# Performance work log

Measured on AMD Instinct MI355X. Metric: run time of the kernel, lower is better.

The kernel has to match this reference:

```python
import jax, jax.numpy as jnp
import numpy as np

D_MODEL = 1024
NUM_HEADS = 16
D_K = D_MODEL // NUM_HEADS


def setup_inputs() -> dict:
    key = jax.random.key(0)
    ks = jax.random.split(key, 11)
    B, S = 2, 2048
    scale = 1.0 / np.sqrt(D_MODEL)
    inp = {
        "query": jax.random.normal(ks[0], (B, S, D_MODEL), jnp.float32),
        "key": jax.random.normal(ks[1], (B, S, D_MODEL), jnp.float32),
        "value": jax.random.normal(ks[2], (B, S, D_MODEL), jnp.float32),
        "Wq": jax.random.normal(ks[3], (D_MODEL, D_MODEL), jnp.float32) * scale,
        "bq": jnp.zeros((D_MODEL,), jnp.float32),
        "Wk": jax.random.normal(ks[4], (D_MODEL, D_MODEL), jnp.float32) * scale,
        "bk": jnp.zeros((D_MODEL,), jnp.float32),
        "Wv": jax.random.normal(ks[5], (D_MODEL, D_MODEL), jnp.float32) * scale,
        "bv": jnp.zeros((D_MODEL,), jnp.float32),
        "Wo": jax.random.normal(ks[6], (D_MODEL, D_MODEL), jnp.float32) * scale,
        "bo": jnp.zeros((D_MODEL,), jnp.float32),
    }
    return inp


def _split_heads(x):
    B, S, _ = x.shape
    return x.reshape(B, S, NUM_HEADS, D_K).transpose(0, 2, 1, 3)  # [B,H,S,d_k]


def reference(query, key, value, Wq, bq, Wk, bk, Wv, bv, Wo, bo):
    # Linear projections (torch Linear: x @ W.T + b)
    q = _split_heads(query @ Wq.T + bq)
    k = _split_heads(key @ Wk.T + bk)
    v = _split_heads(value @ Wv.T + bv)
    scores = jnp.einsum("bhqd,bhkd->bhqk", q, k) / jnp.sqrt(jnp.float32(D_K))
    probs = jax.nn.softmax(scores, axis=-1)
    out = jnp.einsum("bhqk,bhkd->bhqd", probs, v)  # [B,H,S,d_k]
    B, H, S, _ = out.shape
    out = out.transpose(0, 2, 1, 3).reshape(B, S, D_MODEL)
    return out @ Wo.T + bo
```

## Files before the change

### kernel.cpp

```cpp
#include <hip/hip_runtime.h>

#define D_MODEL 1024
#define NHEADS  16
#define DK      64
#define SEQ     2048
#define NBATCH  2
#define MTOT    (NBATCH * SEQ)

typedef _Float16 f16;
typedef _Float16 f16x4 __attribute__((ext_vector_type(4)));
typedef _Float16 f16x8 __attribute__((ext_vector_type(8)));
typedef float    f32x4 __attribute__((ext_vector_type(4)));

__global__ __launch_bounds__(256) void cvt_f32_to_f16(
    const float* __restrict__ q, const float* __restrict__ k, const float* __restrict__ v,
    const float* __restrict__ wq, const float* __restrict__ wk,
    const float* __restrict__ wv, const float* __restrict__ wo,
    f16* __restrict__ qf, f16* __restrict__ kf, f16* __restrict__ vf,
    f16* __restrict__ wqh, f16* __restrict__ wkh, f16* __restrict__ wvh, f16* __restrict__ woh)
{
    const int z = blockIdx.y;
    const float* src; f16* dst; int n4;
    if (z == 0)      { src = q;  dst = qf;  n4 = MTOT * D_MODEL / 4; }
    else if (z == 1) { src = k;  dst = kf;  n4 = MTOT * D_MODEL / 4; }
    else if (z == 2) { src = v;  dst = vf;  n4 = MTOT * D_MODEL / 4; }
    else if (z == 3) { src = wq; dst = wqh; n4 = D_MODEL * D_MODEL / 4; }
    else if (z == 4) { src = wk; dst = wkh; n4 = D_MODEL * D_MODEL / 4; }
    else if (z == 5) { src = wv; dst = wvh; n4 = D_MODEL * D_MODEL / 4; }
    else             { src = wo; dst = woh; n4 = D_MODEL * D_MODEL / 4; }
    for (int i = blockIdx.x * 256 + threadIdx.x; i < n4; i += gridDim.x * 256) {
        float4 t = ((const float4*)src)[i];
        f16x4 o = {(f16)t.x, (f16)t.y, (f16)t.z, (f16)t.w};
        ((f16x4*)dst)[i] = o;
    }
}

__device__ __forceinline__ void gemm128_core(
    const f16* __restrict__ A, const f16* __restrict__ Wm,
    int m0, int n0, f32x4 (&acc)[4][4])
{
    __shared__ __align__(16) f16 As[4096];
    __shared__ __align__(16) f16 Bs[4096];

    const int t    = threadIdx.x;
    const int lane = t & 63;
    const int w    = t >> 6;
    const int quad = lane >> 4, l15 = lane & 15;
    const int wr   = w >> 1,    wc  = w & 1;

    size_t offA[2], offB[2];
#pragma unroll
    for (int jj = 0; jj < 2; ++jj) {
        int s  = (w * 2 + jj) * 64 + lane;
        int ko = s >> 7, m = s & 127;
        offA[jj] = (size_t)(m0 + m) * D_MODEL + ko * 8;
        offB[jj] = (size_t)(n0 + m) * D_MODEL + ko * 8;
    }
    const int jb = __builtin_amdgcn_readfirstlane(w * 2 * 512);

#pragma unroll
    for (int i = 0; i < 4; ++i)
#pragma unroll
        for (int j = 0; j < 4; ++j) acc[i][j] = (f32x4){0.f, 0.f, 0.f, 0.f};

    auto* ldsA = (__attribute__((address_space(3))) f16*)As;
    auto* ldsB = (__attribute__((address_space(3))) f16*)Bs;

    for (int k0 = 0; k0 < D_MODEL; k0 += 32) {
#pragma unroll
        for (int jj = 0; jj < 2; ++jj) {
            __builtin_amdgcn_global_load_lds(
                (const __attribute__((address_space(1))) void*)(A + offA[jj] + k0),
                (__attribute__((address_space(3))) void*)(ldsA + jb + jj * 512),
                16, 0, 0);
            __builtin_amdgcn_global_load_lds(
                (const __attribute__((address_space(1))) void*)(Wm + offB[jj] + k0),
                (__attribute__((address_space(3))) void*)(ldsB + jb + jj * 512),
                16, 0, 0);
        }
        __syncthreads();

        f16x8 af[4], bf[4];
#pragma unroll
        for (int i = 0; i < 4; ++i) {
            af[i] = *(const f16x8*)&As[quad * 1024 + (wr * 64 + i * 16 + l15) * 8];
            bf[i] = *(const f16x8*)&Bs[quad * 1024 + (wc * 64 + i * 16 + l15) * 8];
        }
#pragma unroll
        for (int i = 0; i < 4; ++i)
#pragma unroll
            for (int j = 0; j < 4; ++j)
                acc[i][j] = __builtin_amdgcn_mfma_f32_16x16x32_f16(af[i], bf[j], acc[i][j], 0, 0, 0);
        __syncthreads();
    }
}

__global__ __launch_bounds__(256, 3) void qkv_gemm(
    const f16* __restrict__ Qf, const f16* __restrict__ Kf, const f16* __restrict__ Vf,
    const f16* __restrict__ Wqh, const f16* __restrict__ Wkh, const f16* __restrict__ Wvh,
    const float* __restrict__ bq, const float* __restrict__ bk, const float* __restrict__ bv,
    f16* __restrict__ Qh, f16* __restrict__ Kh, f16* __restrict__ Vt)
{
    const int z = blockIdx.z;
    const f16*   A    = z == 0 ? Qf  : z == 1 ? Kf  : Vf;
    const f16*   Wm   = z == 0 ? Wqh : z == 1 ? Wkh : Wvh;
    const float* bias = z == 0 ? bq  : z == 1 ? bk  : bv;

    const int m0 = blockIdx.y * 128, n0 = blockIdx.x * 128;
    f32x4 acc[4][4];
    gemm128_core(A, Wm, m0, n0, acc);

    const int t = threadIdx.x, lane = t & 63, w = t >> 6;
    const int quad = lane >> 4, l15 = lane & 15;
    const int wr = w >> 1, wc = w & 1;

    if (z < 2) {
        f16* Out = z == 0 ? Qh : Kh;
#pragma unroll
        for (int j = 0; j < 4; ++j) {
            const int col = n0 + wc * 64 + j * 16 + l15;
            const float bc = bias[col];
#pragma unroll
            for (int i = 0; i < 4; ++i)
#pragma unroll
                for (int r = 0; r < 4; ++r) {
                    const int row = m0 + wr * 64 + i * 16 + quad * 4 + r;
                    Out[(size_t)row * D_MODEL + col] = (f16)(acc[i][j][r] + bc);
                }
        }
    } else {
#pragma unroll
        for (int j = 0; j < 4; ++j) {
            const int col = n0 + wc * 64 + j * 16 + l15;
            const float bc = bias[col];
            const int h = col >> 6, d = col & 63;
#pragma unroll
            for (int i = 0; i < 4; ++i)
#pragma unroll
                for (int r = 0; r < 4; ++r) {
                    const int row = m0 + wr * 64 + i * 16 + quad * 4 + r;
                    const int bb = row >> 11, s = row & (SEQ - 1);
                    Vt[(size_t)((bb * NHEADS + h) * DK + d) * SEQ + s] = (f16)(acc[i][j][r] + bc);
                }
        }
    }
}

__global__ __launch_bounds__(256, 3) void oproj_gemm(
    const f16* __restrict__ A, const f16* __restrict__ Wm,
    const float* __restrict__ bias, float* __restrict__ Out)
{
    const int m0 = blockIdx.y * 128, n0 = blockIdx.x * 128;
    f32x4 acc[4][4];
    gemm128_core(A, Wm, m0, n0, acc);

    const int t = threadIdx.x, lane = t & 63, w = t >> 6;
    const int quad = lane >> 4, l15 = lane & 15;
    const int wr = w >> 1, wc = w & 1;
#pragma unroll
    for (int j = 0; j < 4; ++j) {
        const int col = n0 + wc * 64 + j * 16 + l15;
        const float bc = bias[col];
#pragma unroll
        for (int i = 0; i < 4; ++i)
#pragma unroll
            for (int r = 0; r < 4; ++r) {
                const int row = m0 + wr * 64 + i * 16 + quad * 4 + r;
                Out[(size_t)row * D_MODEL + col] = acc[i][j][r] + bc;
            }
    }
}

__global__ __launch_bounds__(256) void mha_mfma_f16(
    const f16* __restrict__ Qh, const f16* __restrict__ Kh,
    const f16* __restrict__ Vt, f16* __restrict__ Og)
{
    __shared__ __align__(16) f16 Qs[64][72];
    __shared__ __align__(16) f16 Ks[64][72];
    __shared__ __align__(16) f16 Vs[64][72];
    __shared__ __align__(16) f16 Ps[64][72];

    const int t    = threadIdx.x;
    const int w    = t >> 6;
    const int lane = t & 63;
    const int quad = lane >> 4;
    const int l15  = lane & 15;

    const int qt = blockIdx.x;
    const int bh = blockIdx.y;
    const int b  = bh >> 4;
    const int h  = bh & 15;
    const int q0 = qt * 64;

    const int r0 = t >> 3;
    const int c0 = (t & 7) * 8;

#pragma unroll
    for (int i = 0; i < 2; ++i) {
        int r = r0 + i * 32;
        *(f16x8*)&Qs[r][c0] =
            *(const f16x8*)&Qh[(size_t)(b * SEQ + q0 + r) * D_MODEL + h * DK + c0];
    }
    __syncthreads();

    const f16x8 aQ0 = *(const f16x8*)&Qs[w * 16 + l15][quad * 8];
    const f16x8 aQ1 = *(const f16x8*)&Qs[w * 16 + l15][32 + quad * 8];

    f32x4 o[4];
#pragma unroll
    for (int f = 0; f < 4; ++f) o[f] = (f32x4){0.f, 0.f, 0.f, 0.f};
    float m_run[4], l_run[4];
#pragma unroll
    for (int r = 0; r < 4; ++r) { m_run[r] = -1e30f; l_run[r] = 0.f; }

    for (int kt = 0; kt < SEQ / 64; ++kt) {
        const int kv0 = kt * 64;
#pragma unroll
        for (int i = 0; i < 2; ++i) {
            int r = r0 + i * 32;
            *(f16x8*)&Ks[r][c0] =
                *(const f16x8*)&Kh[(size_t)(b * SEQ + kv0 + r) * D_MODEL + h * DK + c0];
            *(f16x8*)&Vs[r][c0] =
                *(const f16x8*)&Vt[(size_t)(bh * DK + r) * SEQ + kv0 + c0];
        }
        __syncthreads();

        f32x4 s[4];
#pragma unroll
        for (int f = 0; f < 4; ++f) {
            f16x8 b0 = *(const f16x8*)&Ks[f * 16 + l15][quad * 8];
            f16x8 b1 = *(const f16x8*)&Ks[f * 16 + l15][32 + quad * 8];
            f32x4 a0 = (f32x4){0.f, 0.f, 0.f, 0.f};
            a0 = __builtin_amdgcn_mfma_f32_16x16x32_f16(aQ0, b0, a0, 0, 0, 0);
            a0 = __builtin_amdgcn_mfma_f32_16x16x32_f16(aQ1, b1, a0, 0, 0, 0);
            s[f] = a0;
        }

#pragma unroll
        for (int f = 0; f < 4; ++f)
#pragma unroll
            for (int r = 0; r < 4; ++r) s[f][r] *= 0.125f;

#pragma unroll
        for (int r = 0; r < 4; ++r) {
            float v = fmaxf(fmaxf(s[0][r], s[1][r]), fmaxf(s[2][r], s[3][r]));
            v = fmaxf(v, __shfl_xor(v, 1));
            v = fmaxf(v, __shfl_xor(v, 2));
            v = fmaxf(v, __shfl_xor(v, 4));
            v = fmaxf(v, __shfl_xor(v, 8));
            float mn    = fmaxf(m_run[r], v);
            float alpha = __expf(m_run[r] - mn);
            m_run[r] = mn;
            float rsum = 0.f;
#pragma unroll
            for (int f = 0; f < 4; ++f) {
                float p = __expf(s[f][r] - mn);
                s[f][r] = p;
                rsum += p;
            }
            rsum += __shfl_xor(rsum, 1);
            rsum += __shfl_xor(rsum, 2);
            rsum += __shfl_xor(rsum, 4);
            rsum += __shfl_xor(rsum, 8);
            l_run[r] = l_run[r] * alpha + rsum;
#pragma unroll
            for (int f = 0; f < 4; ++f) o[f][r] *= alpha;
        }

#pragma unroll
        for (int f = 0; f < 4; ++f)
#pragma unroll
            for (int r = 0; r < 4; ++r)
                Ps[w * 16 + quad * 4 + r][f * 16 + l15] = (f16)s[f][r];

        f16x8 aP0 = *(const f16x8*)&Ps[w * 16 + l15][quad * 8];
        f16x8 aP1 = *(const f16x8*)&Ps[w * 16 + l15][32 + quad * 8];
#pragma unroll
        for (int f = 0; f < 4; ++f) {
            f16x8 b0 = *(const f16x8*)&Vs[f * 16 + l15][quad * 8];
            f16x8 b1 = *(const f16x8*)&Vs[f * 16 + l15][32 + quad * 8];
            o[f] = __builtin_amdgcn_mfma_f32_16x16x32_f16(aP0, b0, o[f], 0, 0, 0);
            o[f] = __builtin_amdgcn_mfma_f32_16x16x32_f16(aP1, b1, o[f], 0, 0, 0);
        }
        __syncthreads();
    }

#pragma unroll
    for (int r = 0; r < 4; ++r) {
        const float inv = 1.f / l_run[r];
        const size_t row = (size_t)(b * SEQ + q0 + w * 16 + quad * 4 + r) * D_MODEL + h * DK;
#pragma unroll
        for (int f = 0; f < 4; ++f)
            Og[row + f * 16 + l15] = (f16)(o[f][r] * inv);
    }
}

extern "C" void kernel_launch(void* const* d_in, const int* in_sizes, int n_in,
                              void* d_out, int out_size, void* d_ws, size_t ws_size,
                              hipStream_t stream)
{
    const float* query = (const float*)d_in[0];
    const float* key   = (const float*)d_in[1];
    const float* value = (const float*)d_in[2];
    const float* Wq    = (const float*)d_in[3];
    const float* bq    = (const float*)d_in[4];
    const float* Wk    = (const float*)d_in[5];
    const float* bk    = (const float*)d_in[6];
    const float* Wv    = (const float*)d_in[7];
    const float* bv    = (const float*)d_in[8];
    const float* Wo    = (const float*)d_in[9];
    const float* bo    = (const float*)d_in[10];
    float* out = (float*)d_out;

    f16* Qf  = (f16*)d_ws;
    f16* Kf  = Qf  + (size_t)MTOT * D_MODEL;
    f16* Vf  = Kf  + (size_t)MTOT * D_MODEL;
    f16* Wqh = Vf  + (size_t)MTOT * D_MODEL;
    f16* Wkh = Wqh + (size_t)D_MODEL * D_MODEL;
    f16* Wvh = Wkh + (size_t)D_MODEL * D_MODEL;
    f16* Woh = Wvh + (size_t)D_MODEL * D_MODEL;
    f16* Qh  = Woh + (size_t)D_MODEL * D_MODEL;
    f16* Kh  = Qh  + (size_t)MTOT * D_MODEL;
    f16* Vt  = Kh  + (size_t)MTOT * D_MODEL;
    f16* ATh = Vt  + (size_t)MTOT * D_MODEL;

    cvt_f32_to_f16<<<dim3(1024, 7), 256, 0, stream>>>(
        query, key, value, Wq, Wk, Wv, Wo, Qf, Kf, Vf, Wqh, Wkh, Wvh, Woh);

    qkv_gemm<<<dim3(D_MODEL / 128, MTOT / 128, 3), 256, 0, stream>>>(
        Qf, Kf, Vf, Wqh, Wkh, Wvh, bq, bk, bv, Qh, Kh, Vt);

    mha_mfma_f16<<<dim3(SEQ / 64, NBATCH * NHEADS), 256, 0, stream>>>(Qh, Kh, Vt, ATh);

    oproj_gemm<<<dim3(D_MODEL / 128, MTOT / 128), 256, 0, stream>>>(ATh, Woh, bo, out);
}
```

Measured before the change: 328.2 us.

## Rewrite attention kernel with 128-row Q tiles, direct-to-LDS loads and MFMA row sums

The attention kernel now processes 128 query rows per block, with each wave handling two 16-row subtiles, so every K/V tile loaded into LDS is reused twice as much. K/V tiles are copied with global_load_lds into a chunk-major LDS layout, skipping the register round trip. Row max reductions use DPP instead of shuffles, and the softmax denominator comes from an MFMA against a ones vector rather than shuffle sums. The 1/sqrt(dk) scale is folded into the Q projection epilogue. The cost is more registers per thread and half as many blocks, with launch bounds raised to ask for two blocks per CU.

```diff
diff --git a/kernel.cpp b/kernel.cpp
--- a/kernel.cpp
+++ b/kernel.cpp
@@ -116,6 +116,7 @@
 
     if (z < 2) {
         f16* Out = z == 0 ? Qh : Kh;
+        const float sc = z == 0 ? 0.125f : 1.0f;
 #pragma unroll
         for (int j = 0; j < 4; ++j) {
             const int col = n0 + wc * 64 + j * 16 + l15;
@@ -125,7 +126,7 @@
 #pragma unroll
                 for (int r = 0; r < 4; ++r) {
                     const int row = m0 + wr * 64 + i * 16 + quad * 4 + r;
-                    Out[(size_t)row * D_MODEL + col] = (f16)(acc[i][j][r] + bc);
+                    Out[(size_t)row * D_MODEL + col] = (f16)((acc[i][j][r] + bc) * sc);
                 }
         }
     } else {
@@ -171,128 +172,155 @@
     }
 }
 
-__global__ __launch_bounds__(256) void mha_mfma_f16(
+__device__ __forceinline__ float dpp_max16(float v) {
+    v = fmaxf(v, __uint_as_float(__builtin_amdgcn_update_dpp(
+            0, (int)__float_as_uint(v), 0xB1, 0xF, 0xF, false)));
+    v = fmaxf(v, __uint_as_float(__builtin_amdgcn_update_dpp(
+            0, (int)__float_as_uint(v), 0x4E, 0xF, 0xF, false)));
+    v = fmaxf(v, __uint_as_float(__builtin_amdgcn_update_dpp(
+            0, (int)__float_as_uint(v), 0x141, 0xF, 0xF, false)));
+    v = fmaxf(v, __uint_as_float(__builtin_amdgcn_update_dpp(
+            0, (int)__float_as_uint(v), 0x140, 0xF, 0xF, false)));
+    return v;
+}
+
+__global__ __launch_bounds__(256, 2) void mha_mfma_v3(
     const f16* __restrict__ Qh, const f16* __restrict__ Kh,
     const f16* __restrict__ Vt, f16* __restrict__ Og)
 {
-    __shared__ __align__(16) f16 Qs[64][72];
-    __shared__ __align__(16) f16 Ks[64][72];
-    __shared__ __align__(16) f16 Vs[64][72];
-    __shared__ __align__(16) f16 Ps[64][72];
+    __shared__ __align__(16) f16 Ks[4096];
+    __shared__ __align__(16) f16 Vc[4096];
+    __shared__ __align__(16) f16 Ps[128 * 68];
 
     const int t    = threadIdx.x;
     const int w    = t >> 6;
     const int lane = t & 63;
-    const int quad = lane >> 4;
-    const int l15  = lane & 15;
-
-    const int qt = blockIdx.x;
-    const int bh = blockIdx.y;
-    const int b  = bh >> 4;
-    const int h  = bh & 15;
-    const int q0 = qt * 64;
-
-    const int r0 = t >> 3;
-    const int c0 = (t & 7) * 8;
-
-#pragma unroll
-    for (int i = 0; i < 2; ++i) {
-        int r = r0 + i * 32;
-        *(f16x8*)&Qs[r][c0] =
-            *(const f16x8*)&Qh[(size_t)(b * SEQ + q0 + r) * D_MODEL + h * DK + c0];
-    }
-    __syncthreads();
-
-    const f16x8 aQ0 = *(const f16x8*)&Qs[w * 16 + l15][quad * 8];
-    const f16x8 aQ1 = *(const f16x8*)&Qs[w * 16 + l15][32 + quad * 8];
-
-    f32x4 o[4];
-#pragma unroll
-    for (int f = 0; f < 4; ++f) o[f] = (f32x4){0.f, 0.f, 0.f, 0.f};
-    float m_run[4], l_run[4];
-#pragma unroll
-    for (int r = 0; r < 4; ++r) { m_run[r] = -1e30f; l_run[r] = 0.f; }
+    const int quad = lane >> 4, l15 = lane & 15;
+
+    const int qt = blockIdx.x, bh = blockIdx.y;
+    const int b  = bh >> 4,    h  = bh & 15;
+    const int q0 = qt * 128;
+
+    f16x8 aQ[2][2];
+#pragma unroll
+    for (int s = 0; s < 2; ++s)
+#pragma unroll
+        for (int c = 0; c < 2; ++c)
+            aQ[s][c] = *(const f16x8*)&Qh[
+                (size_t)(b * SEQ + q0 + w * 32 + s * 16 + l15) * D_MODEL
+                + h * DK + c * 32 + quad * 8];
+
+    const f16* gK[2]; const f16* gV[2]; int ldst[2];
+#pragma unroll
+    for (int jj = 0; jj < 2; ++jj) {
+        const int kc = w * 2 + jj;
+        gK[jj] = Kh + (size_t)(b * SEQ + lane) * D_MODEL + h * DK + kc * 8;
+        gV[jj] = Vt + (size_t)(bh * DK + lane) * SEQ + kc * 8;
+        ldst[jj] = __builtin_amdgcn_readfirstlane(kc * 512);
+    }
+    auto* ldsK = (__attribute__((address_space(3))) f16*)Ks;
+    auto* ldsV = (__attribute__((address_space(3))) f16*)Vc;
+
+    const f16x8 onesB = {(f16)1.f, (f16)1.f, (f16)1.f, (f16)1.f,
+                         (f16)1.f, (f16)1.f, (f16)1.f, (f16)1.f};
+
+    f32x4 o[2][4];
+#pragma unroll
+    for (int s = 0; s < 2; ++s)
+#pragma unroll
+        for (int j = 0; j < 4; ++j) o[s][j] = (f32x4){0.f, 0.f, 0.f, 0.f};
+    f32x4 sacc[2] = {(f32x4){0.f, 0.f, 0.f, 0.f}, (f32x4){0.f, 0.f, 0.f, 0.f}};
+    float m_run[2][4];
+#pragma unroll
+    for (int s = 0; s < 2; ++s)
+#pragma unroll
+        for (int r = 0; r < 4; ++r) m_run[s][r] = -1e30f;
 
     for (int kt = 0; kt < SEQ / 64; ++kt) {
-        const int kv0 = kt * 64;
-#pragma unroll
-        for (int i = 0; i < 2; ++i) {
-            int r = r0 + i * 32;
-            *(f16x8*)&Ks[r][c0] =
-                *(const f16x8*)&Kh[(size_t)(b * SEQ + kv0 + r) * D_MODEL + h * DK + c0];
-            *(f16x8*)&Vs[r][c0] =
-                *(const f16x8*)&Vt[(size_t)(bh * DK + r) * SEQ + kv0 + c0];
+#pragma unroll
+        for (int jj = 0; jj < 2; ++jj) {
+            __builtin_amdgcn_global_load_lds(
+                (const __attribute__((address_space(1))) void*)(gK[jj] + (size_t)kt * 64 * D_MODEL),
+                (__attribute__((address_space(3))) void*)(ldsK + ldst[jj]), 16, 0, 0);
+            __builtin_amdgcn_global_load_lds(
+                (const __attribute__((address_space(1))) void*)(gV[jj] + kt * 64),
+                (__attribute__((address_space(3))) void*)(ldsV + ldst[jj]), 16, 0, 0);
         }
         __syncthreads();
 
-        f32x4 s[4];
-#pragma unroll
-        for (int f = 0; f < 4; ++f) {
-            f16x8 b0 = *(const f16x8*)&Ks[f * 16 + l15][quad * 8];
-            f16x8 b1 = *(const f16x8*)&Ks[f * 16 + l15][32 + quad * 8];
-            f32x4 a0 = (f32x4){0.f, 0.f, 0.f, 0.f};
-            a0 = __builtin_amdgcn_mfma_f32_16x16x32_f16(aQ0, b0, a0, 0, 0, 0);
-            a0 = __builtin_amdgcn_mfma_f32_16x16x32_f16(aQ1, b1, a0, 0, 0, 0);
-            s[f] = a0;
-        }
-
+        f16x8 bK[4][2], bV[4][2];
 #pragma unroll
         for (int f = 0; f < 4; ++f)
 #pragma unroll
-            for (int r = 0; r < 4; ++r) s[f][r] *= 0.125f;
-
+            for (int c = 0; c < 2; ++c) {
+                const int slot = ((c * 4 + quad) * 64 + f * 16 + l15) * 8;
+                bK[f][c] = *(const f16x8*)&Ks[slot];
+                bV[f][c] = *(const f16x8*)&Vc[slot];
+            }
+
+#pragma unroll
+        for (int s = 0; s < 2; ++s) {
+            f32x4 sc[4];
+#pragma unroll
+            for (int f = 0; f < 4; ++f) {
+                f32x4 a = (f32x4){0.f, 0.f, 0.f, 0.f};
+                a = __builtin_amdgcn_mfma_f32_16x16x32_f16(aQ[s][0], bK[f][0], a, 0, 0, 0);
+                a = __builtin_amdgcn_mfma_f32_16x16x32_f16(aQ[s][1], bK[f][1], a, 0, 0, 0);
+                sc[f] = a;
+            }
+
+            float al[4];
+#pragma unroll
+            for (int r = 0; r < 4; ++r) {
+                float mt = fmaxf(fmaxf(sc[0][r], sc[1][r]), fmaxf(sc[2][r], sc[3][r]));
+                mt = dpp_max16(mt);
+                const float mn = fmaxf(m_run[s][r], mt);
+                al[r] = __expf(m_run[s][r] - mn);
+                m_run[s][r] = mn;
+#pragma unroll
+                for (int f = 0; f < 4; ++f) sc[f][r] = __expf(sc[f][r] - mn);
+                sacc[s][r] *= al[r];
+#pragma unroll
+                for (int j = 0; j < 4; ++j) o[s][j][r] *= al[r];
+            }
+
+#pragma unroll
+            for (int f = 0; f < 4; ++f)
+#pragma unroll
+                for (int r = 0; r < 4; ++r)
+                    Ps[(w * 32 + s * 16 + quad * 4 + r) * 68 + f * 16 + l15] = (f16)sc[f][r];
+
+            f16x8 aP[2];
+#pragma unroll
+            for (int c = 0; c < 2; ++c) {
+                const int off = (w * 32 + s * 16 + l15) * 68 + c * 32 + quad * 8;
+                f16x4 lo = *(const f16x4*)&Ps[off];
+                f16x4 hi = *(const f16x4*)&Ps[off + 4];
+                aP[c] = __builtin_shufflevector(lo, hi, 0, 1, 2, 3, 4, 5, 6, 7);
+            }
+
+#pragma unroll
+            for (int j = 0; j < 4; ++j) {
+                o[s][j] = __builtin_amdgcn_mfma_f32_16x16x32_f16(aP[0], bV[j][0], o[s][j], 0, 0, 0);
+                o[s][j] = __builtin_amdgcn_mfma_f32_16x16x32_f16(aP[1], bV[j][1], o[s][j], 0, 0, 0);
+            }
+            sacc[s] = __builtin_amdgcn_mfma_f32_16x16x32_f16(aP[0], onesB, sacc[s], 0, 0, 0);
+            sacc[s] = __builtin_amdgcn_mfma_f32_16x16x32_f16(aP[1], onesB, sacc[s], 0, 0, 0);
+        }
+        __syncthreads();
+    }
+
+#pragma unroll
+    for (int s = 0; s < 2; ++s)
 #pragma unroll
         for (int r = 0; r < 4; ++r) {
-            float v = fmaxf(fmaxf(s[0][r], s[1][r]), fmaxf(s[2][r], s[3][r]));
-            v = fmaxf(v, __shfl_xor(v, 1));
-            v = fmaxf(v, __shfl_xor(v, 2));
-            v = fmaxf(v, __shfl_xor(v, 4));
-            v = fmaxf(v, __shfl_xor(v, 8));
-            float mn    = fmaxf(m_run[r], v);
-            float alpha = __expf(m_run[r] - mn);
-            m_run[r] = mn;
-            float rsum = 0.f;
-#pragma unroll
-            for (int f = 0; f < 4; ++f) {
-                float p = __expf(s[f][r] - mn);
-                s[f][r] = p;
-                rsum += p;
-            }
-            rsum += __shfl_xor(rsum, 1);
-            rsum += __shfl_xor(rsum, 2);
-            rsum += __shfl_xor(rsum, 4);
-            rsum += __shfl_xor(rsum, 8);
-            l_run[r] = l_run[r] * alpha + rsum;
-#pragma unroll
-            for (int f = 0; f < 4; ++f) o[f][r] *= alpha;
-        }
-
-#pragma unroll
-        for (int f = 0; f < 4; ++f)
-#pragma unroll
-            for (int r = 0; r < 4; ++r)
-                Ps[w * 16 + quad * 4 + r][f * 16 + l15] = (f16)s[f][r];
-
-        f16x8 aP0 = *(const f16x8*)&Ps[w * 16 + l15][quad * 8];
-        f16x8 aP1 = *(const f16x8*)&Ps[w * 16 + l15][32 + quad * 8];
-#pragma unroll
-        for (int f = 0; f < 4; ++f) {
-            f16x8 b0 = *(const f16x8*)&Vs[f * 16 + l15][quad * 8];
-            f16x8 b1 = *(const f16x8*)&Vs[f * 16 + l15][32 + quad * 8];
-            o[f] = __builtin_amdgcn_mfma_f32_16x16x32_f16(aP0, b0, o[f], 0, 0, 0);
-            o[f] = __builtin_amdgcn_mfma_f32_16x16x32_f16(aP1, b1, o[f], 0, 0, 0);
-        }
-        __syncthreads();
-    }
-
-#pragma unroll
-    for (int r = 0; r < 4; ++r) {
-        const float inv = 1.f / l_run[r];
-        const size_t row = (size_t)(b * SEQ + q0 + w * 16 + quad * 4 + r) * D_MODEL + h * DK;
-#pragma unroll
-        for (int f = 0; f < 4; ++f)
-            Og[row + f * 16 + l15] = (f16)(o[f][r] * inv);
-    }
+            const float inv = 1.f / sacc[s][r];
+            const size_t row = (size_t)(b * SEQ + q0 + w * 32 + s * 16 + quad * 4 + r) * D_MODEL
+                               + h * DK;
+#pragma unroll
+            for (int j = 0; j < 4; ++j)
+                Og[row + j * 16 + l15] = (f16)(o[s][j][r] * inv);
+        }
 }
 
 extern "C" void kernel_launch(void* const* d_in, const int* in_sizes, int n_in,
@@ -330,7 +358,7 @@
     qkv_gemm<<<dim3(D_MODEL / 128, MTOT / 128, 3), 256, 0, stream>>>(
         Qf, Kf, Vf, Wqh, Wkh, Wvh, bq, bk, bv, Qh, Kh, Vt);
 
-    mha_mfma_f16<<<dim3(SEQ / 64, NBATCH * NHEADS), 256, 0, stream>>>(Qh, Kh, Vt, ATh);
+    mha_mfma_v3<<<dim3(SEQ / 128, NBATCH * NHEADS), 256, 0, stream>>>(Qh, Kh, Vt, ATh);
 
     oproj_gemm<<<dim3(D_MODEL / 128, MTOT / 128), 256, 0, stream>>>(ATh, Woh, bo, out);
 }
```

Result: faster. 289.2 us (-11.9%).
